# Performance work log

Measured on AMD Instinct MI355X. Metric: run time of the kernel, lower is better.

## Reference

```python
import jax, jax.numpy as jnp
import numpy as np

H, D, EF, NT, ET = 4, 32, 32, 4, 8
N, E = 100000, 1600000
NEG_SLOPE = 0.2


def setup_inputs() -> dict:
    key = jax.random.key(0)
    ks = jax.random.split(key, 11)
    return {
        "feat": jax.random.normal(ks[0], (N, H * D), jnp.float32),
        "fc": jax.random.normal(ks[1], (NT, H, D), jnp.float32) * 0.1,
        "edge_emb": jax.random.normal(ks[2], (ET, EF), jnp.float32),
        "W_e": jax.random.normal(ks[3], (H * EF, EF), jnp.float32) * 0.1,
        "attn_l": jax.random.normal(ks[4], (1, H, D), jnp.float32) * 0.1,
        "attn_r": jax.random.normal(ks[5], (1, H, D), jnp.float32) * 0.1,
        "attn_e": jax.random.normal(ks[6], (1, H, EF), jnp.float32) * 0.1,
        "node_types": jax.random.randint(ks[7], (N,), 0, NT, jnp.int32),
        "e_feat": jax.random.randint(ks[8], (E,), 0, ET, jnp.int32),
        "src": jax.random.randint(ks[9], (E,), 0, N, jnp.int32),
        "dst": jax.random.randint(ks[10], (E,), 0, N, jnp.int32),
    }


def reference(feat, fc, edge_emb, W_e, attn_l, attn_r, attn_e, node_types, e_feat, src, dst):
    n = feat.shape[0]
    h = feat.reshape(n, H, D)                      # [N,H,D] (h_src == h_dst)
    fs = h * fc[node_types]                        # per-node-type scaling, feat_src == feat_dst

    # edge-type embedding path: Embedding -> Linear(edge_feats, H*edge_feats) -> attn_e score
    emb = (edge_emb @ W_e.T).reshape(ET, H, EF)    # [ET,H,EF]
    ee = (emb * attn_e).sum(-1)[e_feat]            # [E,H]

    el = (fs * attn_l).sum(-1)                     # [N,H]
    er = (fs * attn_r).sum(-1)                     # [N,H]
    e = jax.nn.leaky_relu(el[src] + er[dst] + ee, NEG_SLOPE)  # [E,H]

    # edge_softmax: segment softmax over destination node
    m = jax.ops.segment_max(e, dst, num_segments=n)           # [N,H]
    ex = jnp.exp(e - m[dst])
    s = jax.ops.segment_sum(ex, dst, num_segments=n)          # [N,H]
    a = ex / s[dst]                                            # [E,H]

    # u_mul_e + sum aggregation
    msg = fs[src] * a[:, :, None]                              # [E,H,D]
    rst = jax.ops.segment_sum(msg, dst, num_segments=n)       # [N,H,D]

    rst = rst + h                                              # residual (Identity, in==out feats)
    return rst, a[:, :, None]
```

## Files before the change

kernel.cpp:

```cpp
#include <hip/hip_runtime.h>
#include <stdint.h>

namespace {
constexpr int kH = 4, kD = 32, kEF = 32, kNT = 4, kET = 8;
constexpr int kHD = kH * kD;
constexpr float kNegSlope = 0.2f;
constexpr int kNB = 782;
constexpr int kHB = 512;
constexpr int kXP = 20;

using f32x2 = __attribute__((ext_vector_type(2))) float;

__device__ __forceinline__ float lrelu(float x) { return x > 0.f ? x : kNegSlope * x; }

__global__ void __launch_bounds__(256) k_init(
    const float* __restrict__ feat, const float* __restrict__ fc,
    const float* __restrict__ edge_emb, const float* __restrict__ W_e,
    const float* __restrict__ attn_l, const float* __restrict__ attn_r,
    const float* __restrict__ attn_e, const int* __restrict__ node_types,
    float* __restrict__ el, float* __restrict__ er, uint8_t* __restrict__ fs,
    float* __restrict__ ee_tab, int N) {
  if (blockIdx.x == 0 && threadIdx.x < kET * kH) {
    int et = threadIdx.x / kH, h = threadIdx.x % kH;
    float acc = 0.f;
    for (int f = 0; f < kEF; ++f) {
      const float* wrow = W_e + (h * kEF + f) * kEF;
      const float* erow = edge_emb + et * kEF;
      float emb = 0.f;
      for (int k = 0; k < kEF; ++k) emb += erow[k] * wrow[k];
      acc += emb * attn_e[h * kEF + f];
    }
    ee_tab[et * kH + h] = acc;
  }
  int gid = blockIdx.x * blockDim.x + threadIdx.x;
  int node = gid >> 5;
  int lane = threadIdx.x & 31;
  if (node >= N) return;
  int nt = node_types[node];
  float4 f4 = *(const float4*)(feat + (size_t)(node << 7) + lane * 4);
  float4 c4 = *(const float4*)(fc + nt * kHD + lane * 4);
  float4 al = *(const float4*)(attn_l + lane * 4);
  float4 ar = *(const float4*)(attn_r + lane * 4);
  float fx = f4.x * c4.x, fy = f4.y * c4.y, fz = f4.z * c4.z, fw = f4.w * c4.w;
  int w = __builtin_amdgcn_cvt_pk_fp8_f32(fx, fy, 0, false);
  w = __builtin_amdgcn_cvt_pk_fp8_f32(fz, fw, w, true);
  *(int*)(fs + (size_t)(node << 7) + lane * 4) = w;
  float pl = fx * al.x + fy * al.y + fz * al.z + fw * al.w;
  float pr = fx * ar.x + fy * ar.y + fz * ar.z + fw * ar.w;
#pragma unroll
  for (int off = 1; off < 8; off <<= 1) {
    pl += __shfl_xor(pl, off);
    pr += __shfl_xor(pr, off);
  }
  if ((lane & 7) == 0) {
    int h = lane >> 3;
    el[node * kH + h] = pl;
    er[node * kH + h] = pr;
  }
}

__global__ void __launch_bounds__(256) k_hist(const int* __restrict__ dst,
                                              int* __restrict__ partial, int E) {
  __shared__ int h[kNB];
  for (int i = threadIdx.x; i < kNB; i += 256) h[i] = 0;
  __syncthreads();
  int per = (E + gridDim.x - 1) / gridDim.x;
  int e0 = blockIdx.x * per;
  int e1 = min(e0 + per, E);
  for (int i = e0 + threadIdx.x; i < e1; i += 256) atomicAdd(&h[dst[i] >> 7], 1);
  __syncthreads();
  for (int i = threadIdx.x; i < kNB; i += 256) partial[blockIdx.x * kNB + i] = h[i];
}

__global__ void __launch_bounds__(256) k_scanA(int* __restrict__ partial,
                                               int* __restrict__ btot) {
  __shared__ int bufa[kHB], bufb[kHB];
  int b = blockIdx.x, t = threadIdx.x;
  bufa[t] = partial[t * kNB + b];
  bufa[t + 256] = partial[(t + 256) * kNB + b];
  __syncthreads();
  int* cur = bufa;
  int* nxt = bufb;
  for (int off = 1; off < kHB; off <<= 1) {
    for (int i = t; i < kHB; i += 256) nxt[i] = cur[i] + (i >= off ? cur[i - off] : 0);
    __syncthreads();
    int* sw = cur; cur = nxt; nxt = sw;
  }
  partial[t * kNB + b] = t ? cur[t - 1] : 0;
  partial[(t + 256) * kNB + b] = cur[t + 255];
  if (t == 0) btot[b] = cur[kHB - 1];
}

__global__ void __launch_bounds__(1024) k_scanB(const int* __restrict__ btot,
                                                int* __restrict__ bbase) {
  __shared__ int bufa[1024], bufb[1024];
  int t = threadIdx.x;
  bufa[t] = (t < kNB) ? btot[t] : 0;
  __syncthreads();
  int* cur = bufa;
  int* nxt = bufb;
  for (int off = 1; off < 1024; off <<= 1) {
    nxt[t] = cur[t] + (t >= off ? cur[t - off] : 0);
    __syncthreads();
    int* sw = cur; cur = nxt; nxt = sw;
  }
  if (t < kNB) bbase[t] = t ? cur[t - 1] : 0;
  if (t == kNB - 1) bbase[kNB] = cur[t];
}

__global__ void __launch_bounds__(256) k_scatter2(
    const int* __restrict__ dst, const int* __restrict__ src,
    const int* __restrict__ e_feat, const int* __restrict__ partial,
    const int* __restrict__ bbase, int* __restrict__ tmp, int E) {
  __shared__ int h[kNB];
  for (int i = threadIdx.x; i < kNB; i += 256) h[i] = 0;
  __syncthreads();
  int per = (E + gridDim.x - 1) / gridDim.x;
  int e0 = blockIdx.x * per;
  int e1 = min(e0 + per, E);
  const int* myrow = partial + blockIdx.x * kNB;
  for (int i = e0 + threadIdx.x; i < e1; i += 256) {
    int d = dst[i];
    int b = d >> 7;
    int lr = atomicAdd(&h[b], 1);
    int pos = bbase[b] + myrow[b] + lr;
    tmp[pos] = src[i] | (e_feat[i] << 17) | ((d & 127) << 20);
  }
}

__global__ void __launch_bounds__(256) k_build(const int* __restrict__ bbase,
                                               const int* __restrict__ tmp,
                                               int* __restrict__ ptr,
                                               int* __restrict__ csr, int N, int E) {
  __shared__ int fh[128], fb[128], sc[128];
  int b = blockIdx.x, t = threadIdx.x;
  int s0 = bbase[b], s1 = bbase[b + 1];
  if (t < 128) fh[t] = 0;
  __syncthreads();
  for (int j = s0 + t; j < s1; j += 256) atomicAdd(&fh[tmp[j] >> 20], 1);
  __syncthreads();
  if (t < 128) sc[t] = fh[t];
  __syncthreads();
  for (int off = 1; off < 128; off <<= 1) {
    int v = 0;
    if (t < 128 && t >= off) v = sc[t - off];
    __syncthreads();
    if (t < 128) sc[t] += v;
    __syncthreads();
  }
  if (t < 128) {
    fb[t] = sc[t] - fh[t];
    int d = (b << 7) + t;
    if (d < N) ptr[d] = s0 + fb[t];
    fh[t] = 0;
  }
  if (b == gridDim.x - 1 && t == 0) ptr[N] = E;
  __syncthreads();
  for (int j = s0 + t; j < s1; j += 256) {
    int v = tmp[j];
    int dl = v >> 20;
    int r = atomicAdd(&fh[dl], 1);
    csr[s0 + fb[dl] + r] = v & 0xFFFFF;
  }
}

__global__ void __launch_bounds__(256) k_fused(
    const uint8_t* __restrict__ fs, const float* __restrict__ feat,
    const float* __restrict__ el, const float* __restrict__ er,
    const float* __restrict__ ee_tab, const int* __restrict__ ptr,
    const int* __restrict__ csr, float* __restrict__ rst,
    float* __restrict__ rinv_buf, int N) {
  __shared__ float ee_sh[kET * kH];
  __shared__ __align__(16) float xp[4][64 * kXP];
  if (threadIdx.x < kET * kH) ee_sh[threadIdx.x] = ee_tab[threadIdx.x];
  __syncthreads();
  int lane = threadIdx.x & 63;
  int wid = threadIdx.x >> 6;
  int node = blockIdx.x * 4 + wid;
  bool nvalid = node < N;
  int nodec = nvalid ? node : 0;
  int start = 0, end = 0;
  if (nvalid) {
    start = ptr[node];
    end = ptr[node + 1];
  }

  int g = lane >> 3;
  int q = lane & 7;
  int head = q >> 1;
  int qoff = q << 4;
  float er_h = er[nodec * kH + head];

  float sm = 0.f;
  f32x2 acc[8];
#pragma unroll
  for (int k = 0; k < 8; ++k) acc[k] = (f32x2){0.f, 0.f};

  int j = start + g;
  int pk0 = csr[(j < end) ? j : 0];
  int s0 = pk0 & 0x1FFFF;
  float elv0 = el[(s0 << 2) + head];
  int4 w0 = *(const int4*)(fs + (size_t)(s0 << 7) + qoff);
  float ee0 = ee_sh[((pk0 >> 17) << 2) + head];
  int pk1 = csr[(j + 8 < end) ? j + 8 : 0];

  while (j < end) {
    int s1 = pk1 & 0x1FFFF;
    float elv1 = el[(s1 << 2) + head];
    int4 w1 = *(const int4*)(fs + (size_t)(s1 << 7) + qoff);
    float ee1 = ee_sh[((pk1 >> 17) << 2) + head];
    int pk2 = csr[(j + 16 < end) ? j + 16 : 0];
    float ex = __expf(lrelu(elv0 + er_h + ee0));
    sm += ex;
    f32x2 ex2 = {ex, ex};
#pragma unroll
    for (int c = 0; c < 4; ++c) {
      int wc = c == 0 ? w0.x : c == 1 ? w0.y : c == 2 ? w0.z : w0.w;
      acc[2 * c + 0] += ex2 * __builtin_amdgcn_cvt_pk_f32_fp8(wc, false);
      acc[2 * c + 1] += ex2 * __builtin_amdgcn_cvt_pk_f32_fp8(wc, true);
    }
    elv0 = elv1;
    w0 = w1;
    ee0 = ee1;
    pk1 = pk2;
    j += 8;
  }

  sm += __shfl_xor(sm, 8);
  sm += __shfl_xor(sm, 16);
  sm += __shfl_xor(sm, 32);
  float rinv = sm > 0.f ? 1.f / sm : 0.f;

  float* row = &xp[wid][lane * kXP];
#pragma unroll
  for (int c = 0; c < 4; ++c) {
    float4 v4 = {acc[2 * c].x, acc[2 * c].y, acc[2 * c + 1].x, acc[2 * c + 1].y};
    *(float4*)(row + c * 4) = v4;
  }
  __syncthreads();
  int qsrc = lane >> 3;
  int coff = (lane & 7) * 2;
  const float* base = &xp[wid][qsrc * kXP + coff];
  f32x2 v = {0.f, 0.f};
#pragma unroll
  for (int gg = 0; gg < 8; ++gg) v += *(const f32x2*)(base + gg * 8 * kXP);

  float rs = __shfl(rinv, (lane >> 4) << 1);
  float rb = __shfl(rinv, lane << 1);
  f32x2 f2 = *(const f32x2*)(feat + (size_t)(nodec << 7) + lane * 2);
  f32x2 o = v * rs + f2;
  if (nvalid) {
    *(f32x2*)(rst + (size_t)(node << 7) + lane * 2) = o;
    if (lane < kH) rinv_buf[node * kH + lane] = rb;
  }
}

__global__ void k_post(const int* __restrict__ src, const int* __restrict__ dst,
                       const int* __restrict__ e_feat, const float* __restrict__ el,
                       const float* __restrict__ er, const float* __restrict__ ee_tab,
                       const float* __restrict__ rinv_buf, float* __restrict__ out_a,
                       int E) {
  int i = blockIdx.x * blockDim.x + threadIdx.x;
  if (i >= E) return;
  int s = src[i], d = dst[i], et = e_feat[i];
  float4 elv = *(const float4*)(el + s * kH);
  float4 erv = *(const float4*)(er + d * kH);
  float4 ee = *(const float4*)(ee_tab + et * kH);
  float4 rv = *(const float4*)(rinv_buf + d * kH);
  float4 a;
  a.x = __expf(lrelu(elv.x + erv.x + ee.x)) * rv.x;
  a.y = __expf(lrelu(elv.y + erv.y + ee.y)) * rv.y;
  a.z = __expf(lrelu(elv.z + erv.z + ee.z)) * rv.z;
  a.w = __expf(lrelu(elv.w + erv.w + ee.w)) * rv.w;
  *(float4*)(out_a + (size_t)i * kH) = a;
}

}

extern "C" void kernel_launch(void* const* d_in, const int* in_sizes, int n_in,
                              void* d_out, int out_size, void* d_ws, size_t ws_size,
                              hipStream_t stream) {
  const float* feat = (const float*)d_in[0];
  const float* fc = (const float*)d_in[1];
  const float* edge_emb = (const float*)d_in[2];
  const float* W_e = (const float*)d_in[3];
  const float* attn_l = (const float*)d_in[4];
  const float* attn_r = (const float*)d_in[5];
  const float* attn_e = (const float*)d_in[6];
  const int* node_types = (const int*)d_in[7];
  const int* e_feat = (const int*)d_in[8];
  const int* src = (const int*)d_in[9];
  const int* dst = (const int*)d_in[10];
  int N = in_sizes[7];
  int E = in_sizes[8];

  char* ws = (char*)d_ws;
  size_t off = 0;
  auto alloc = [&](size_t bytes) -> void* {
    void* p = ws + off;
    off = (off + bytes + 255) & ~(size_t)255;
    return p;
  };
  float* ee_tab = (float*)alloc((size_t)kET * kH * sizeof(float));
  float* el = (float*)alloc((size_t)N * kH * sizeof(float));
  float* er = (float*)alloc((size_t)N * kH * sizeof(float));
  float* rinv_buf = (float*)alloc((size_t)N * kH * sizeof(float));
  uint8_t* fs = (uint8_t*)alloc((size_t)N * kHD * sizeof(uint8_t));
  int* partial = (int*)alloc((size_t)kHB * kNB * sizeof(int));
  int* btot = (int*)alloc((size_t)kNB * sizeof(int));
  int* bbase = (int*)alloc((size_t)(kNB + 1) * sizeof(int));
  int* ptr = (int*)alloc((size_t)(N + 1) * sizeof(int));
  int* tmp = (int*)alloc((size_t)E * sizeof(int));
  int* csr = (int*)alloc((size_t)E * sizeof(int));

  k_init<<<(N + 7) / 8, 256, 0, stream>>>(feat, fc, edge_emb, W_e, attn_l, attn_r,
                                          attn_e, node_types, el, er, fs, ee_tab, N);
  k_hist<<<kHB, 256, 0, stream>>>(dst, partial, E);
  k_scanA<<<kNB, 256, 0, stream>>>(partial, btot);
  k_scanB<<<1, 1024, 0, stream>>>(btot, bbase);
  k_scatter2<<<kHB, 256, 0, stream>>>(dst, src, e_feat, partial, bbase, tmp, E);
  k_build<<<kNB, 256, 0, stream>>>(bbase, tmp, ptr, csr, N, E);

  float* rst = (float*)d_out;
  float* out_a = (float*)d_out + (size_t)N * kHD;
  k_fused<<<(N + 3) / 4, 256, 0, stream>>>(fs, feat, el, er, ee_tab, ptr, csr, rst,
                                           rinv_buf, N);
  k_post<<<(E + 255) / 256, 256, 0, stream>>>(src, dst, e_feat, el, er, ee_tab,
                                              rinv_buf, out_a, E);
}
```

Measured before the change: 307.3 us.

## Build CSR with global atomic degree counts instead of two-level bucket sort

Replaces the five-kernel CSR build (block histogram, two scans, bucket scatter, per-bucket local sort) with a degree count fused into the init kernel, a single per-block scan over degrees, and a placement kernel that uses global atomics per destination. This removes several launches and the intermediate tmp pass, but relies on contended global atomics and yields nondeterministic edge order within each node. The fused kernel also deepens its gather prefetch pipeline by one stage and hoists the residual feature load to the top.

```diff
diff --git a/kernel.cpp b/kernel.cpp
--- a/kernel.cpp
+++ b/kernel.cpp
@@ -5,8 +5,6 @@
 constexpr int kH = 4, kD = 32, kEF = 32, kNT = 4, kET = 8;
 constexpr int kHD = kH * kD;
 constexpr float kNegSlope = 0.2f;
-constexpr int kNB = 782;
-constexpr int kHB = 512;
 constexpr int kXP = 20;
 
 using f32x2 = __attribute__((ext_vector_type(2))) float;
@@ -18,8 +16,11 @@
     const float* __restrict__ edge_emb, const float* __restrict__ W_e,
     const float* __restrict__ attn_l, const float* __restrict__ attn_r,
     const float* __restrict__ attn_e, const int* __restrict__ node_types,
+    const int* __restrict__ dst, int* __restrict__ deg,
     float* __restrict__ el, float* __restrict__ er, uint8_t* __restrict__ fs,
-    float* __restrict__ ee_tab, int N) {
+    float* __restrict__ ee_tab, int N, int E) {
+  int gid = blockIdx.x * blockDim.x + threadIdx.x;
+  if (gid < E) atomicAdd(&deg[dst[gid]], 1);
   if (blockIdx.x == 0 && threadIdx.x < kET * kH) {
     int et = threadIdx.x / kH, h = threadIdx.x % kH;
     float acc = 0.f;
@@ -32,7 +33,6 @@
     }
     ee_tab[et * kH + h] = acc;
   }
-  int gid = blockIdx.x * blockDim.x + threadIdx.x;
   int node = gid >> 5;
   int lane = threadIdx.x & 31;
   if (node >= N) return;
@@ -59,108 +59,53 @@
   }
 }
 
-__global__ void __launch_bounds__(256) k_hist(const int* __restrict__ dst,
-                                              int* __restrict__ partial, int E) {
-  __shared__ int h[kNB];
-  for (int i = threadIdx.x; i < kNB; i += 256) h[i] = 0;
-  __syncthreads();
+__global__ void __launch_bounds__(1024) k_scan(const int* __restrict__ deg,
+                                               int* __restrict__ ptr,
+                                               int* __restrict__ wcnt, int N) {
+  __shared__ int sa[1024], sb[1024];
+  int b = blockIdx.x, t = threadIdx.x;
+  int hi = b << 10;
+  int acc = 0;
+  for (int i = t; i < hi; i += 1024) acc += deg[i];
+  sa[t] = acc;
+  __syncthreads();
+  for (int off = 512; off > 0; off >>= 1) {
+    if (t < off) sa[t] += sa[t + off];
+    __syncthreads();
+  }
+  int base = sa[0];
+  __syncthreads();
+  int i = hi + t;
+  int v = (i < N) ? deg[i] : 0;
+  sa[t] = v;
+  __syncthreads();
+  int* cur = sa;
+  int* nxt = sb;
+  for (int off = 1; off < 1024; off <<= 1) {
+    nxt[t] = cur[t] + ((t >= off) ? cur[t - off] : 0);
+    __syncthreads();
+    int* sw = cur; cur = nxt; nxt = sw;
+  }
+  int excl = base + cur[t] - v;
+  if (i < N) {
+    ptr[i] = excl;
+    wcnt[i] = excl;
+  }
+  if (i == N) ptr[N] = excl;
+}
+
+__global__ void __launch_bounds__(256) k_place(const int* __restrict__ dst,
+                                               const int* __restrict__ src,
+                                               const int* __restrict__ e_feat,
+                                               int* __restrict__ wcnt,
+                                               int* __restrict__ csr, int E) {
   int per = (E + gridDim.x - 1) / gridDim.x;
   int e0 = blockIdx.x * per;
   int e1 = min(e0 + per, E);
-  for (int i = e0 + threadIdx.x; i < e1; i += 256) atomicAdd(&h[dst[i] >> 7], 1);
-  __syncthreads();
-  for (int i = threadIdx.x; i < kNB; i += 256) partial[blockIdx.x * kNB + i] = h[i];
-}
-
-__global__ void __launch_bounds__(256) k_scanA(int* __restrict__ partial,
-                                               int* __restrict__ btot) {
-  __shared__ int bufa[kHB], bufb[kHB];
-  int b = blockIdx.x, t = threadIdx.x;
-  bufa[t] = partial[t * kNB + b];
-  bufa[t + 256] = partial[(t + 256) * kNB + b];
-  __syncthreads();
-  int* cur = bufa;
-  int* nxt = bufb;
-  for (int off = 1; off < kHB; off <<= 1) {
-    for (int i = t; i < kHB; i += 256) nxt[i] = cur[i] + (i >= off ? cur[i - off] : 0);
-    __syncthreads();
-    int* sw = cur; cur = nxt; nxt = sw;
-  }
-  partial[t * kNB + b] = t ? cur[t - 1] : 0;
-  partial[(t + 256) * kNB + b] = cur[t + 255];
-  if (t == 0) btot[b] = cur[kHB - 1];
-}
-
-__global__ void __launch_bounds__(1024) k_scanB(const int* __restrict__ btot,
-                                                int* __restrict__ bbase) {
-  __shared__ int bufa[1024], bufb[1024];
-  int t = threadIdx.x;
-  bufa[t] = (t < kNB) ? btot[t] : 0;
-  __syncthreads();
-  int* cur = bufa;
-  int* nxt = bufb;
-  for (int off = 1; off < 1024; off <<= 1) {
-    nxt[t] = cur[t] + (t >= off ? cur[t - off] : 0);
-    __syncthreads();
-    int* sw = cur; cur = nxt; nxt = sw;
-  }
-  if (t < kNB) bbase[t] = t ? cur[t - 1] : 0;
-  if (t == kNB - 1) bbase[kNB] = cur[t];
-}
-
-__global__ void __launch_bounds__(256) k_scatter2(
-    const int* __restrict__ dst, const int* __restrict__ src,
-    const int* __restrict__ e_feat, const int* __restrict__ partial,
-    const int* __restrict__ bbase, int* __restrict__ tmp, int E) {
-  __shared__ int h[kNB];
-  for (int i = threadIdx.x; i < kNB; i += 256) h[i] = 0;
-  __syncthreads();
-  int per = (E + gridDim.x - 1) / gridDim.x;
-  int e0 = blockIdx.x * per;
-  int e1 = min(e0 + per, E);
-  const int* myrow = partial + blockIdx.x * kNB;
   for (int i = e0 + threadIdx.x; i < e1; i += 256) {
     int d = dst[i];
-    int b = d >> 7;
-    int lr = atomicAdd(&h[b], 1);
-    int pos = bbase[b] + myrow[b] + lr;
-    tmp[pos] = src[i] | (e_feat[i] << 17) | ((d & 127) << 20);
-  }
-}
-
-__global__ void __launch_bounds__(256) k_build(const int* __restrict__ bbase,
-                                               const int* __restrict__ tmp,
-                                               int* __restrict__ ptr,
-                                               int* __restrict__ csr, int N, int E) {
-  __shared__ int fh[128], fb[128], sc[128];
-  int b = blockIdx.x, t = threadIdx.x;
-  int s0 = bbase[b], s1 = bbase[b + 1];
-  if (t < 128) fh[t] = 0;
-  __syncthreads();
-  for (int j = s0 + t; j < s1; j += 256) atomicAdd(&fh[tmp[j] >> 20], 1);
-  __syncthreads();
-  if (t < 128) sc[t] = fh[t];
-  __syncthreads();
-  for (int off = 1; off < 128; off <<= 1) {
-    int v = 0;
-    if (t < 128 && t >= off) v = sc[t - off];
-    __syncthreads();
-    if (t < 128) sc[t] += v;
-    __syncthreads();
-  }
-  if (t < 128) {
-    fb[t] = sc[t] - fh[t];
-    int d = (b << 7) + t;
-    if (d < N) ptr[d] = s0 + fb[t];
-    fh[t] = 0;
-  }
-  if (b == gridDim.x - 1 && t == 0) ptr[N] = E;
-  __syncthreads();
-  for (int j = s0 + t; j < s1; j += 256) {
-    int v = tmp[j];
-    int dl = v >> 20;
-    int r = atomicAdd(&fh[dl], 1);
-    csr[s0 + fb[dl] + r] = v & 0xFFFFF;
+    int r = atomicAdd(&wcnt[d], 1);
+    csr[r] = src[i] | (e_feat[i] << 17);
   }
 }
 
@@ -190,6 +135,7 @@
   int head = q >> 1;
   int qoff = q << 4;
   float er_h = er[nodec * kH + head];
+  f32x2 f2 = *(const f32x2*)(feat + (size_t)(nodec << 7) + lane * 2);
 
   float sm = 0.f;
   f32x2 acc[8];
@@ -198,18 +144,23 @@
 
   int j = start + g;
   int pk0 = csr[(j < end) ? j : 0];
+  int pk1 = csr[(j + 8 < end) ? j + 8 : 0];
   int s0 = pk0 & 0x1FFFF;
   float elv0 = el[(s0 << 2) + head];
   int4 w0 = *(const int4*)(fs + (size_t)(s0 << 7) + qoff);
   float ee0 = ee_sh[((pk0 >> 17) << 2) + head];
-  int pk1 = csr[(j + 8 < end) ? j + 8 : 0];
+  int s1 = pk1 & 0x1FFFF;
+  float elv1 = el[(s1 << 2) + head];
+  int4 w1 = *(const int4*)(fs + (size_t)(s1 << 7) + qoff);
+  float ee1 = ee_sh[((pk1 >> 17) << 2) + head];
+  int pk2 = csr[(j + 16 < end) ? j + 16 : 0];
 
   while (j < end) {
-    int s1 = pk1 & 0x1FFFF;
-    float elv1 = el[(s1 << 2) + head];
-    int4 w1 = *(const int4*)(fs + (size_t)(s1 << 7) + qoff);
-    float ee1 = ee_sh[((pk1 >> 17) << 2) + head];
-    int pk2 = csr[(j + 16 < end) ? j + 16 : 0];
+    int s2 = pk2 & 0x1FFFF;
+    float elv2 = el[(s2 << 2) + head];
+    int4 w2 = *(const int4*)(fs + (size_t)(s2 << 7) + qoff);
+    float ee2 = ee_sh[((pk2 >> 17) << 2) + head];
+    int pk3 = csr[(j + 24 < end) ? j + 24 : 0];
     float ex = __expf(lrelu(elv0 + er_h + ee0));
     sm += ex;
     f32x2 ex2 = {ex, ex};
@@ -219,10 +170,9 @@
       acc[2 * c + 0] += ex2 * __builtin_amdgcn_cvt_pk_f32_fp8(wc, false);
       acc[2 * c + 1] += ex2 * __builtin_amdgcn_cvt_pk_f32_fp8(wc, true);
     }
-    elv0 = elv1;
-    w0 = w1;
-    ee0 = ee1;
-    pk1 = pk2;
+    elv0 = elv1; w0 = w1; ee0 = ee1;
+    elv1 = elv2; w1 = w2; ee1 = ee2;
+    pk2 = pk3;
     j += 8;
   }
 
@@ -247,7 +197,6 @@
 
   float rs = __shfl(rinv, (lane >> 4) << 1);
   float rb = __shfl(rinv, lane << 1);
-  f32x2 f2 = *(const f32x2*)(feat + (size_t)(nodec << 7) + lane * 2);
   f32x2 o = v * rs + f2;
   if (nvalid) {
     *(f32x2*)(rst + (size_t)(node << 7) + lane * 2) = o;
@@ -306,20 +255,18 @@
   float* er = (float*)alloc((size_t)N * kH * sizeof(float));
   float* rinv_buf = (float*)alloc((size_t)N * kH * sizeof(float));
   uint8_t* fs = (uint8_t*)alloc((size_t)N * kHD * sizeof(uint8_t));
-  int* partial = (int*)alloc((size_t)kHB * kNB * sizeof(int));
-  int* btot = (int*)alloc((size_t)kNB * sizeof(int));
-  int* bbase = (int*)alloc((size_t)(kNB + 1) * sizeof(int));
+  int* deg = (int*)alloc((size_t)N * sizeof(int));
   int* ptr = (int*)alloc((size_t)(N + 1) * sizeof(int));
-  int* tmp = (int*)alloc((size_t)E * sizeof(int));
+  int* wcnt = (int*)alloc((size_t)N * sizeof(int));
   int* csr = (int*)alloc((size_t)E * sizeof(int));
 
+  hipMemsetAsync(deg, 0, (size_t)N * sizeof(int), stream);
   k_init<<<(N + 7) / 8, 256, 0, stream>>>(feat, fc, edge_emb, W_e, attn_l, attn_r,
-                                          attn_e, node_types, el, er, fs, ee_tab, N);
-  k_hist<<<kHB, 256, 0, stream>>>(dst, partial, E);
-  k_scanA<<<kNB, 256, 0, stream>>>(partial, btot);
-  k_scanB<<<1, 1024, 0, stream>>>(btot, bbase);
-  k_scatter2<<<kHB, 256, 0, stream>>>(dst, src, e_feat, partial, bbase, tmp, E);
-  k_build<<<kNB, 256, 0, stream>>>(bbase, tmp, ptr, csr, N, E);
+                                          attn_e, node_types, dst, deg, el, er, fs,
+                                          ee_tab, N, E);
+  int nscan = (N >> 10) + 1;
+  k_scan<<<nscan, 1024, 0, stream>>>(deg, ptr, wcnt, N);
+  k_place<<<512, 256, 0, stream>>>(dst, src, e_feat, wcnt, csr, E);
 
   float* rst = (float*)d_out;
   float* out_a = (float*)d_out + (size_t)N * kHD;
```

New measurement: 423.4 us. +37.8%, slower.

## Fuse CSR bucket build into aggregation kernel using shared-memory edge lists

Applied to the files above, without the earlier changes.

Drops the separate k_build kernel. Each aggregation block now takes one 64-node bucket, counting-sorts its edges by local destination into shared memory, and processes 16 nodes per wavefront with a deeper three-stage software prefetch. This removes the global CSR write and re-read and one kernel launch. Buckets larger than the shared capacity spill to a global buffer. Bucket size and the histogram block count and width also change, and the per-node syncthreads is replaced by a wave-local waitcnt, which risks load imbalance from fewer, larger blocks.

```diff
diff --git a/kernel.cpp b/kernel.cpp
--- a/kernel.cpp
+++ b/kernel.cpp
@@ -5,8 +5,10 @@
 constexpr int kH = 4, kD = 32, kEF = 32, kNT = 4, kET = 8;
 constexpr int kHD = kH * kD;
 constexpr float kNegSlope = 0.2f;
-constexpr int kNB = 782;
-constexpr int kHB = 512;
+constexpr int kBN = 64;
+constexpr int kNB = (100000 + kBN - 1) / kBN;
+constexpr int kHB = 128;
+constexpr int kCap = 1536;
 constexpr int kXP = 20;
 
 using f32x2 = __attribute__((ext_vector_type(2))) float;
@@ -59,199 +61,219 @@
   }
 }
 
-__global__ void __launch_bounds__(256) k_hist(const int* __restrict__ dst,
+__global__ void __launch_bounds__(512) k_hist(const int* __restrict__ dst,
                                               int* __restrict__ partial, int E) {
   __shared__ int h[kNB];
-  for (int i = threadIdx.x; i < kNB; i += 256) h[i] = 0;
+  for (int i = threadIdx.x; i < kNB; i += 512) h[i] = 0;
   __syncthreads();
   int per = (E + gridDim.x - 1) / gridDim.x;
   int e0 = blockIdx.x * per;
   int e1 = min(e0 + per, E);
-  for (int i = e0 + threadIdx.x; i < e1; i += 256) atomicAdd(&h[dst[i] >> 7], 1);
-  __syncthreads();
-  for (int i = threadIdx.x; i < kNB; i += 256) partial[blockIdx.x * kNB + i] = h[i];
-}
-
-__global__ void __launch_bounds__(256) k_scanA(int* __restrict__ partial,
+  for (int i = e0 + threadIdx.x; i < e1; i += 512) atomicAdd(&h[dst[i] >> 6], 1);
+  __syncthreads();
+  for (int i = threadIdx.x; i < kNB; i += 512) partial[blockIdx.x * kNB + i] = h[i];
+}
+
+__global__ void __launch_bounds__(kHB) k_scanA(int* __restrict__ partial,
                                                int* __restrict__ btot) {
   __shared__ int bufa[kHB], bufb[kHB];
   int b = blockIdx.x, t = threadIdx.x;
-  bufa[t] = partial[t * kNB + b];
-  bufa[t + 256] = partial[(t + 256) * kNB + b];
+  int v = partial[t * kNB + b];
+  bufa[t] = v;
   __syncthreads();
   int* cur = bufa;
   int* nxt = bufb;
   for (int off = 1; off < kHB; off <<= 1) {
-    for (int i = t; i < kHB; i += 256) nxt[i] = cur[i] + (i >= off ? cur[i - off] : 0);
+    nxt[t] = cur[t] + (t >= off ? cur[t - off] : 0);
     __syncthreads();
     int* sw = cur; cur = nxt; nxt = sw;
   }
-  partial[t * kNB + b] = t ? cur[t - 1] : 0;
-  partial[(t + 256) * kNB + b] = cur[t + 255];
-  if (t == 0) btot[b] = cur[kHB - 1];
+  partial[t * kNB + b] = cur[t] - v;
+  if (t == kHB - 1) btot[b] = cur[t];
 }
 
 __global__ void __launch_bounds__(1024) k_scanB(const int* __restrict__ btot,
                                                 int* __restrict__ bbase) {
-  __shared__ int bufa[1024], bufb[1024];
+  __shared__ int sa[1024], sb[1024];
   int t = threadIdx.x;
-  bufa[t] = (t < kNB) ? btot[t] : 0;
-  __syncthreads();
-  int* cur = bufa;
-  int* nxt = bufb;
+  int i0 = 2 * t, i1 = 2 * t + 1;
+  int v0 = (i0 < kNB) ? btot[i0] : 0;
+  int v1 = (i1 < kNB) ? btot[i1] : 0;
+  sa[t] = v0 + v1;
+  __syncthreads();
+  int* cur = sa;
+  int* nxt = sb;
   for (int off = 1; off < 1024; off <<= 1) {
     nxt[t] = cur[t] + (t >= off ? cur[t - off] : 0);
     __syncthreads();
     int* sw = cur; cur = nxt; nxt = sw;
   }
-  if (t < kNB) bbase[t] = t ? cur[t - 1] : 0;
-  if (t == kNB - 1) bbase[kNB] = cur[t];
-}
-
-__global__ void __launch_bounds__(256) k_scatter2(
+  int excl = t ? cur[t - 1] : 0;
+  if (i0 < kNB) bbase[i0] = excl;
+  if (i1 < kNB) bbase[i1] = excl + v0;
+  if (t == 1023) bbase[kNB] = cur[1023];
+}
+
+__global__ void __launch_bounds__(512) k_scatter2(
     const int* __restrict__ dst, const int* __restrict__ src,
     const int* __restrict__ e_feat, const int* __restrict__ partial,
     const int* __restrict__ bbase, int* __restrict__ tmp, int E) {
   __shared__ int h[kNB];
-  for (int i = threadIdx.x; i < kNB; i += 256) h[i] = 0;
+  for (int i = threadIdx.x; i < kNB; i += 512) h[i] = 0;
   __syncthreads();
   int per = (E + gridDim.x - 1) / gridDim.x;
   int e0 = blockIdx.x * per;
   int e1 = min(e0 + per, E);
   const int* myrow = partial + blockIdx.x * kNB;
-  for (int i = e0 + threadIdx.x; i < e1; i += 256) {
+  for (int i = e0 + threadIdx.x; i < e1; i += 512) {
     int d = dst[i];
-    int b = d >> 7;
+    int b = d >> 6;
     int lr = atomicAdd(&h[b], 1);
     int pos = bbase[b] + myrow[b] + lr;
-    tmp[pos] = src[i] | (e_feat[i] << 17) | ((d & 127) << 20);
-  }
-}
-
-__global__ void __launch_bounds__(256) k_build(const int* __restrict__ bbase,
-                                               const int* __restrict__ tmp,
-                                               int* __restrict__ ptr,
-                                               int* __restrict__ csr, int N, int E) {
-  __shared__ int fh[128], fb[128], sc[128];
-  int b = blockIdx.x, t = threadIdx.x;
-  int s0 = bbase[b], s1 = bbase[b + 1];
-  if (t < 128) fh[t] = 0;
-  __syncthreads();
-  for (int j = s0 + t; j < s1; j += 256) atomicAdd(&fh[tmp[j] >> 20], 1);
-  __syncthreads();
-  if (t < 128) sc[t] = fh[t];
-  __syncthreads();
-  for (int off = 1; off < 128; off <<= 1) {
-    int v = 0;
-    if (t < 128 && t >= off) v = sc[t - off];
-    __syncthreads();
-    if (t < 128) sc[t] += v;
-    __syncthreads();
-  }
-  if (t < 128) {
-    fb[t] = sc[t] - fh[t];
-    int d = (b << 7) + t;
-    if (d < N) ptr[d] = s0 + fb[t];
-    fh[t] = 0;
-  }
-  if (b == gridDim.x - 1 && t == 0) ptr[N] = E;
-  __syncthreads();
-  for (int j = s0 + t; j < s1; j += 256) {
-    int v = tmp[j];
-    int dl = v >> 20;
-    int r = atomicAdd(&fh[dl], 1);
-    csr[s0 + fb[dl] + r] = v & 0xFFFFF;
-  }
-}
-
-__global__ void __launch_bounds__(256) k_fused(
+    tmp[pos] = src[i] | (e_feat[i] << 17) | ((d & 63) << 20);
+  }
+}
+
+__global__ void __launch_bounds__(256) k_fused2(
     const uint8_t* __restrict__ fs, const float* __restrict__ feat,
     const float* __restrict__ el, const float* __restrict__ er,
-    const float* __restrict__ ee_tab, const int* __restrict__ ptr,
-    const int* __restrict__ csr, float* __restrict__ rst,
-    float* __restrict__ rinv_buf, int N) {
+    const float* __restrict__ ee_tab, const int* __restrict__ bbase,
+    const int* __restrict__ tmp, int* __restrict__ spare,
+    float* __restrict__ rst, float* __restrict__ rinv_buf, int N) {
   __shared__ float ee_sh[kET * kH];
+  __shared__ int elist[kCap];
+  __shared__ int fh[kBN], fb[kBN + 1], sc[kBN];
   __shared__ __align__(16) float xp[4][64 * kXP];
-  if (threadIdx.x < kET * kH) ee_sh[threadIdx.x] = ee_tab[threadIdx.x];
-  __syncthreads();
+  int t = threadIdx.x;
+  int b = blockIdx.x;
+  int s0 = bbase[b], s1 = bbase[b + 1];
+  int cnt = s1 - s0;
+  if (t < kET * kH) ee_sh[t] = ee_tab[t];
+  if (t < kBN) fh[t] = 0;
+  if (t == 0) elist[0] = 0;
+  __syncthreads();
+  for (int j = s0 + t; j < s1; j += 256) atomicAdd(&fh[(tmp[j] >> 20) & 63], 1);
+  __syncthreads();
+  if (t < kBN) sc[t] = fh[t];
+  __syncthreads();
+  for (int off = 1; off < kBN; off <<= 1) {
+    int v = 0;
+    if (t < kBN && t >= off) v = sc[t - off];
+    __syncthreads();
+    if (t < kBN) sc[t] += v;
+    __syncthreads();
+  }
+  if (t < kBN) {
+    fb[t] = sc[t] - fh[t];
+    fh[t] = 0;
+  }
+  if (t == 0) fb[kBN] = cnt;
+  __syncthreads();
+  bool ovf = cnt > kCap;
+  if (!ovf) {
+    for (int j = s0 + t; j < s1; j += 256) {
+      int v = tmp[j];
+      int dl = (v >> 20) & 63;
+      int r = atomicAdd(&fh[dl], 1);
+      elist[fb[dl] + r] = v;
+    }
+  } else {
+    for (int j = s0 + t; j < s1; j += 256) {
+      int v = tmp[j];
+      int dl = (v >> 20) & 63;
+      int r = atomicAdd(&fh[dl], 1);
+      spare[s0 + fb[dl] + r] = v;
+    }
+  }
+  __syncthreads();
+
   int lane = threadIdx.x & 63;
   int wid = threadIdx.x >> 6;
-  int node = blockIdx.x * 4 + wid;
-  bool nvalid = node < N;
-  int nodec = nvalid ? node : 0;
-  int start = 0, end = 0;
-  if (nvalid) {
-    start = ptr[node];
-    end = ptr[node + 1];
-  }
-
   int g = lane >> 3;
   int q = lane & 7;
   int head = q >> 1;
   int qoff = q << 4;
-  float er_h = er[nodec * kH + head];
-
-  float sm = 0.f;
-  f32x2 acc[8];
-#pragma unroll
-  for (int k = 0; k < 8; ++k) acc[k] = (f32x2){0.f, 0.f};
-
-  int j = start + g;
-  int pk0 = csr[(j < end) ? j : 0];
-  int s0 = pk0 & 0x1FFFF;
-  float elv0 = el[(s0 << 2) + head];
-  int4 w0 = *(const int4*)(fs + (size_t)(s0 << 7) + qoff);
-  float ee0 = ee_sh[((pk0 >> 17) << 2) + head];
-  int pk1 = csr[(j + 8 < end) ? j + 8 : 0];
-
-  while (j < end) {
-    int s1 = pk1 & 0x1FFFF;
-    float elv1 = el[(s1 << 2) + head];
-    int4 w1 = *(const int4*)(fs + (size_t)(s1 << 7) + qoff);
-    float ee1 = ee_sh[((pk1 >> 17) << 2) + head];
-    int pk2 = csr[(j + 16 < end) ? j + 16 : 0];
-    float ex = __expf(lrelu(elv0 + er_h + ee0));
-    sm += ex;
-    f32x2 ex2 = {ex, ex};
-#pragma unroll
-    for (int c = 0; c < 4; ++c) {
-      int wc = c == 0 ? w0.x : c == 1 ? w0.y : c == 2 ? w0.z : w0.w;
-      acc[2 * c + 0] += ex2 * __builtin_amdgcn_cvt_pk_f32_fp8(wc, false);
-      acc[2 * c + 1] += ex2 * __builtin_amdgcn_cvt_pk_f32_fp8(wc, true);
+  float* row = &xp[wid][lane * kXP];
+
+  auto run = [&](const int* eptr) {
+#pragma unroll 1
+    for (int i = 0; i < 16; ++i) {
+      int dl = (wid << 4) + i;
+      int d = (b << 6) + dl;
+      if (d >= N) break;
+      int a0 = fb[dl], a1 = fb[dl + 1];
+      float er_h = er[(d << 2) + head];
+      f32x2 f2 = *(const f32x2*)(feat + ((size_t)d << 7) + lane * 2);
+      float sm = 0.f;
+      f32x2 acc[8];
+#pragma unroll
+      for (int k = 0; k < 8; ++k) acc[k] = (f32x2){0.f, 0.f};
+
+      int j = a0 + g;
+      int pk0 = eptr[(j < a1) ? j : 0];
+      int pk1 = eptr[(j + 8 < a1) ? j + 8 : 0];
+      int ss0 = pk0 & 0x1FFFF;
+      float elv0 = el[(ss0 << 2) + head];
+      int4 w0 = *(const int4*)(fs + ((size_t)ss0 << 7) + qoff);
+      float ee0 = ee_sh[(((pk0 >> 17) & 7) << 2) + head];
+      int ss1 = pk1 & 0x1FFFF;
+      float elv1 = el[(ss1 << 2) + head];
+      int4 w1 = *(const int4*)(fs + ((size_t)ss1 << 7) + qoff);
+      float ee1 = ee_sh[(((pk1 >> 17) & 7) << 2) + head];
+      int pk2 = eptr[(j + 16 < a1) ? j + 16 : 0];
+
+      while (j < a1) {
+        int ss2 = pk2 & 0x1FFFF;
+        float elv2 = el[(ss2 << 2) + head];
+        int4 w2 = *(const int4*)(fs + ((size_t)ss2 << 7) + qoff);
+        float ee2 = ee_sh[(((pk2 >> 17) & 7) << 2) + head];
+        int pk3 = eptr[(j + 24 < a1) ? j + 24 : 0];
+        float ex = __expf(lrelu(elv0 + er_h + ee0));
+        sm += ex;
+        f32x2 ex2 = {ex, ex};
+#pragma unroll
+        for (int c = 0; c < 4; ++c) {
+          int wc = c == 0 ? w0.x : c == 1 ? w0.y : c == 2 ? w0.z : w0.w;
+          acc[2 * c + 0] += ex2 * __builtin_amdgcn_cvt_pk_f32_fp8(wc, false);
+          acc[2 * c + 1] += ex2 * __builtin_amdgcn_cvt_pk_f32_fp8(wc, true);
+        }
+        elv0 = elv1; w0 = w1; ee0 = ee1;
+        elv1 = elv2; w1 = w2; ee1 = ee2;
+        pk2 = pk3;
+        j += 8;
+      }
+
+      sm += __shfl_xor(sm, 8);
+      sm += __shfl_xor(sm, 16);
+      sm += __shfl_xor(sm, 32);
+      float rinv = sm > 0.f ? 1.f / sm : 0.f;
+
+#pragma unroll
+      for (int c = 0; c < 4; ++c) {
+        float4 v4 = {acc[2 * c].x, acc[2 * c].y, acc[2 * c + 1].x, acc[2 * c + 1].y};
+        *(float4*)(row + c * 4) = v4;
+      }
+      asm volatile("s_waitcnt lgkmcnt(0)" ::: "memory");
+      __builtin_amdgcn_sched_barrier(0);
+      int qsrc = lane >> 3;
+      int coff = (lane & 7) * 2;
+      const float* base = &xp[wid][qsrc * kXP + coff];
+      f32x2 v = {0.f, 0.f};
+#pragma unroll
+      for (int gg = 0; gg < 8; ++gg) v += *(const f32x2*)(base + gg * 8 * kXP);
+
+      float rs = __shfl(rinv, (lane >> 4) << 1);
+      float rb = __shfl(rinv, lane << 1);
+      f32x2 o = v * rs + f2;
+      *(f32x2*)(rst + ((size_t)d << 7) + lane * 2) = o;
+      if (lane < kH) rinv_buf[d * kH + lane] = rb;
     }
-    elv0 = elv1;
-    w0 = w1;
-    ee0 = ee1;
-    pk1 = pk2;
-    j += 8;
-  }
-
-  sm += __shfl_xor(sm, 8);
-  sm += __shfl_xor(sm, 16);
-  sm += __shfl_xor(sm, 32);
-  float rinv = sm > 0.f ? 1.f / sm : 0.f;
-
-  float* row = &xp[wid][lane * kXP];
-#pragma unroll
-  for (int c = 0; c < 4; ++c) {
-    float4 v4 = {acc[2 * c].x, acc[2 * c].y, acc[2 * c + 1].x, acc[2 * c + 1].y};
-    *(float4*)(row + c * 4) = v4;
-  }
-  __syncthreads();
-  int qsrc = lane >> 3;
-  int coff = (lane & 7) * 2;
-  const float* base = &xp[wid][qsrc * kXP + coff];
-  f32x2 v = {0.f, 0.f};
-#pragma unroll
-  for (int gg = 0; gg < 8; ++gg) v += *(const f32x2*)(base + gg * 8 * kXP);
-
-  float rs = __shfl(rinv, (lane >> 4) << 1);
-  float rb = __shfl(rinv, lane << 1);
-  f32x2 f2 = *(const f32x2*)(feat + (size_t)(nodec << 7) + lane * 2);
-  f32x2 o = v * rs + f2;
-  if (nvalid) {
-    *(f32x2*)(rst + (size_t)(node << 7) + lane * 2) = o;
-    if (lane < kH) rinv_buf[node * kH + lane] = rb;
+  };
+
+  if (!ovf) {
+    run((const int*)elist);
+  } else {
+    run((const int*)(spare + s0));
   }
 }
 
@@ -309,22 +331,20 @@
   int* partial = (int*)alloc((size_t)kHB * kNB * sizeof(int));
   int* btot = (int*)alloc((size_t)kNB * sizeof(int));
   int* bbase = (int*)alloc((size_t)(kNB + 1) * sizeof(int));
-  int* ptr = (int*)alloc((size_t)(N + 1) * sizeof(int));
   int* tmp = (int*)alloc((size_t)E * sizeof(int));
-  int* csr = (int*)alloc((size_t)E * sizeof(int));
+  int* spare = (int*)alloc((size_t)E * sizeof(int));
 
   k_init<<<(N + 7) / 8, 256, 0, stream>>>(feat, fc, edge_emb, W_e, attn_l, attn_r,
                                           attn_e, node_types, el, er, fs, ee_tab, N);
-  k_hist<<<kHB, 256, 0, stream>>>(dst, partial, E);
-  k_scanA<<<kNB, 256, 0, stream>>>(partial, btot);
+  k_hist<<<kHB, 512, 0, stream>>>(dst, partial, E);
+  k_scanA<<<kNB, kHB, 0, stream>>>(partial, btot);
   k_scanB<<<1, 1024, 0, stream>>>(btot, bbase);
-  k_scatter2<<<kHB, 256, 0, stream>>>(dst, src, e_feat, partial, bbase, tmp, E);
-  k_build<<<kNB, 256, 0, stream>>>(bbase, tmp, ptr, csr, N, E);
+  k_scatter2<<<kHB, 512, 0, stream>>>(dst, src, e_feat, partial, bbase, tmp, E);
 
   float* rst = (float*)d_out;
   float* out_a = (float*)d_out + (size_t)N * kHD;
-  k_fused<<<(N + 3) / 4, 256, 0, stream>>>(fs, feat, el, er, ee_tab, ptr, csr, rst,
-                                           rinv_buf, N);
+  k_fused2<<<kNB, 256, 0, stream>>>(fs, feat, el, er, ee_tab, bbase, tmp, spare,
+                                    rst, rinv_buf, N);
   k_post<<<(E + 255) / 256, 256, 0, stream>>>(src, dst, e_feat, el, er, ee_tab,
                                               rinv_buf, out_a, E);
 }
```

Result: slower. 319.7 us (+4.0%).
